# Optimization experiments

Measured on AMD Instinct MI355X. Metric: run time of the kernel, lower is better.

## Reference

```python
import jax, jax.numpy as jnp
import numpy as np

N = 4096; TD = 768; ID = 512; H = 256; NH = 4; HD = H // NH; NC = 3; E = 131072


def _gcn(x, w, b, src, dst, n):
    # GCNConv: add self loops, sym-normalize, aggregate at dst
    loop = jnp.arange(n)
    s = jnp.concatenate([src, loop])
    d = jnp.concatenate([dst, loop])
    deg = jax.ops.segment_sum(jnp.ones(s.shape[0], x.dtype), d, num_segments=n)
    dinv = jnp.where(deg > 0, jax.lax.rsqrt(deg), 0.0)
    norm = dinv[s] * dinv[d]                      # [E+N]
    h = x @ w                                     # [N,H] transform
    out = jax.ops.segment_sum(norm[:, None] * h[s], d, num_segments=n)
    return out + b


def setup_inputs() -> dict:
    key = jax.random.key(0)
    ks = jax.random.split(key, 20)
    p = lambda k, shp, sc: jax.random.normal(k, shp, jnp.float32) * sc
    inp = {
        "text_features": jax.random.normal(ks[0], (N, TD), jnp.float32),
        "image_features": jax.random.normal(ks[1], (N, ID), jnp.float32),
        "edge_index": jax.random.randint(ks[2], (2, E), 0, N, jnp.int32),
        "text_w": p(ks[3], (TD, H), 0.02), "text_b": jnp.zeros((H,), jnp.float32),
        "image_w": p(ks[4], (ID, H), 0.02), "image_b": jnp.zeros((H,), jnp.float32),
        "wq": p(ks[5], (H, H), 0.02), "bq": jnp.zeros((H,), jnp.float32),
        "wk": p(ks[6], (H, H), 0.02), "bk": jnp.zeros((H,), jnp.float32),
        "wv": p(ks[7], (H, H), 0.02), "bv": jnp.zeros((H,), jnp.float32),
        "wo": p(ks[8], (H, H), 0.02), "bo": jnp.zeros((H,), jnp.float32),
        "gcn1_w": p(ks[9], (H, H), 0.02), "gcn1_b": jnp.zeros((H,), jnp.float32),
        "gcn2_w": p(ks[10], (H, H), 0.02), "gcn2_b": jnp.zeros((H,), jnp.float32),
        "cls_w": p(ks[11], (H, NC), 0.02), "cls_b": jnp.zeros((NC,), jnp.float32),
    }
    return inp


def reference(text_features, image_features, edge_index,
              text_w, text_b, image_w, image_b,
              wq, bq, wk, bk, wv, bv, wo, bo,
              gcn1_w, gcn1_b, gcn2_w, gcn2_b, cls_w, cls_b):
    # fused linear+relu projections, then elementwise fuse of sum
    combined = (jax.nn.relu(text_features @ text_w + text_b)
                + jax.nn.relu(image_features @ image_w + image_b))  # [N,H]
    # MHA over all nodes (seq_len=N, batch=1)
    q = (combined @ wq + bq).reshape(N, NH, HD)
    k = (combined @ wk + bk).reshape(N, NH, HD)
    v = (combined @ wv + bv).reshape(N, NH, HD)
    scores = jnp.einsum('nhd,mhd->hnm', q, k) / jnp.sqrt(jnp.float32(HD))
    attn = jax.nn.softmax(scores, axis=-1)
    o = jnp.einsum('hnm,mhd->nhd', attn, v).reshape(N, H)
    attn_out = o @ wo + bo
    # two GCN layers
    src, dst = edge_index[0], edge_index[1]
    g1 = jax.nn.relu(_gcn(attn_out, gcn1_w, gcn1_b, src, dst, N))
    g2 = _gcn(g1, gcn2_w, gcn2_b, src, dst, N)
    return g2 @ cls_w + cls_b
```

## Files before the change

### kernel.cpp

```cpp
#include <hip/hip_runtime.h>
#include <hip/hip_bf16.h>

typedef unsigned short ushort;
typedef __attribute__((ext_vector_type(8))) short short8;
typedef __attribute__((ext_vector_type(4))) short short4v;
typedef __attribute__((ext_vector_type(4))) float f32x4;

constexpr int N_  = 4096;
constexpr int TD_ = 768;
constexpr int ID_ = 512;
constexpr int H_  = 256;
constexpr int HD_ = 64;
constexpr int E_  = 131072;
constexpr int SPLITS = 8;
constexpr float QSCALE = 0.125f * 1.44269504088896f;

#define MFMA16(a, b, c) __builtin_amdgcn_mfma_f32_16x16x32_bf16(a, b, c, 0, 0, 0)

__device__ inline ushort f2bf(float x) {
    union { float f; unsigned u; } v; v.f = x;
    unsigned r = v.u + 0x7fff + ((v.u >> 16) & 1);
    return (ushort)(r >> 16);
}
__device__ inline float lo2f(unsigned u) { union { unsigned x; float f; } v; v.x = u << 16; return v.f; }
__device__ inline float hi2f(unsigned u) { union { unsigned x; float f; } v; v.x = u & 0xffff0000u; return v.f; }

__device__ inline float exp2r(float x) {
    float r;
    asm("v_exp_f32 %0, %1" : "=v"(r) : "v"(x));
    return r;
}
__device__ inline unsigned pkbf(float lo, float hi) {
    union { float f; unsigned u; } a, b; a.f = lo; b.f = hi;
    return __builtin_amdgcn_perm(b.u + 0x8000u, a.u + 0x8000u, 0x07060302u);
}

__device__ inline void gl_lds16(const void* g, void* l) {
    __builtin_amdgcn_global_load_lds((const __attribute__((address_space(1))) unsigned int*)g,
                                     (__attribute__((address_space(3))) unsigned int*)l, 16, 0, 0);
}

__device__ inline void stage64(const ushort* g, long long strideEl, ushort* lds, int w, int l) {
    int r8 = l >> 3;
    int cc = (l & 7) ^ r8;
    #pragma unroll
    for (int p = 0; p < 2; p++) {
        int row = w * 16 + p * 8 + r8;
        gl_lds16(g + (long long)row * strideEl + cc * 8, lds + (w * 16 + p * 8) * 64);
    }
}
__device__ inline int swz(int row, int kOff) {
    return row * 64 + ((((kOff >> 3) ^ (row & 7))) << 3);
}


__global__ __launch_bounds__(256) void k_init(int* __restrict__ indeg, int* __restrict__ pos) {
    int i = blockIdx.x * 256 + threadIdx.x;
    indeg[i] = 0;
    pos[i] = 0;
}

__global__ __launch_bounds__(256) void k_count(const int* __restrict__ dst, int* __restrict__ indeg) {
    int e = blockIdx.x * 256 + threadIdx.x;
    atomicAdd(&indeg[dst[e]], 1);
}

__global__ __launch_bounds__(1024) void k_scan(const int* __restrict__ indeg, int* __restrict__ offs,
                                               float* __restrict__ dinv) {
    __shared__ int sums[1024];
    int t = threadIdx.x;
    int b = t * 4;
    int a0 = indeg[b], a1 = indeg[b + 1], a2 = indeg[b + 2], a3 = indeg[b + 3];
    int s = a0 + a1 + a2 + a3;
    sums[t] = s;
    __syncthreads();
    for (int off = 1; off < 1024; off <<= 1) {
        int vv = (t >= off) ? sums[t - off] : 0;
        __syncthreads();
        sums[t] += vv;
        __syncthreads();
    }
    int excl = sums[t] - s;
    offs[b]     = excl;
    offs[b + 1] = excl + a0;
    offs[b + 2] = excl + a0 + a1;
    offs[b + 3] = excl + a0 + a1 + a2;
    dinv[b]     = 1.f / sqrtf((float)(a0 + 1));
    dinv[b + 1] = 1.f / sqrtf((float)(a1 + 1));
    dinv[b + 2] = 1.f / sqrtf((float)(a2 + 1));
    dinv[b + 3] = 1.f / sqrtf((float)(a3 + 1));
}

__global__ __launch_bounds__(256) void k_scatter(const int* __restrict__ src, const int* __restrict__ dst,
                                                 const int* __restrict__ offs, const float* __restrict__ dinv,
                                                 int* __restrict__ pos, int* __restrict__ ssrc,
                                                 float* __restrict__ sw) {
    int e = blockIdx.x * 256 + threadIdx.x;
    int s = src[e], d = dst[e];
    int p = atomicAdd(&pos[d], 1);
    int idx = offs[d] + p;
    ssrc[idx] = s;
    sw[idx] = dinv[s] * dinv[d];
}


__global__ __launch_bounds__(256) void k_prep(const float* __restrict__ text, const float* __restrict__ img,
                                              const float* __restrict__ tw, const float* __restrict__ iw,
                                              const float* __restrict__ wq, const float* __restrict__ wk,
                                              const float* __restrict__ wv, const float* __restrict__ wo,
                                              const float* __restrict__ g1w, const float* __restrict__ g2w,
                                              ushort* __restrict__ textbf, ushort* __restrict__ imgbf,
                                              ushort* __restrict__ wobf,
                                              ushort* __restrict__ twT, ushort* __restrict__ iwT,
                                              ushort* __restrict__ wqT, ushort* __restrict__ wkT,
                                              ushort* __restrict__ wvT, ushort* __restrict__ g1wT,
                                              ushort* __restrict__ g2wT) {
    __shared__ float Ts[64][65];
    const int b = blockIdx.x;
    const int t = threadIdx.x;
    if (b < 2592) {
        size_t base = ((size_t)b * 256 + t) * 8;
        const size_t TXE = (size_t)N_ * TD_, IME = (size_t)N_ * ID_;
        const float* src; ushort* dst;
        if (base < TXE) { src = text + base; dst = textbf + base; }
        else if (base < TXE + IME) { src = img + (base - TXE); dst = imgbf + (base - TXE); }
        else { src = wo + (base - TXE - IME); dst = wobf + (base - TXE - IME); }
        float4 x = *(const float4*)src;
        float4 y = *(const float4*)(src + 4);
        ushort o[8] = { f2bf(x.x), f2bf(x.y), f2bf(x.z), f2bf(x.w),
                        f2bf(y.x), f2bf(y.y), f2bf(y.z), f2bf(y.w) };
        *(short8*)dst = *(const short8*)o;
        return;
    }
    int wb = b - 2592;
    const float* src; ushort* dst; int R, tile;
    if (wb < 48)       { src = tw;  dst = twT;  R = 768; tile = wb; }
    else if (wb < 80)  { src = iw;  dst = iwT;  R = 512; tile = wb - 48; }
    else if (wb < 96)  { src = wq;  dst = wqT;  R = 256; tile = wb - 80; }
    else if (wb < 112) { src = wk;  dst = wkT;  R = 256; tile = wb - 96; }
    else if (wb < 128) { src = wv;  dst = wvT;  R = 256; tile = wb - 112; }
    else if (wb < 144) { src = g1w; dst = g1wT; R = 256; tile = wb - 128; }
    else               { src = g2w; dst = g2wT; R = 256; tile = wb - 144; }
    const int r0 = (tile >> 2) * 64, c0 = (tile & 3) * 64;
    #pragma unroll
    for (int u = 0; u < 16; u++) {
        int lin = t + u * 256;
        int r = lin >> 6, c = lin & 63;
        Ts[r][c] = src[(size_t)(r0 + r) * 256 + c0 + c];
    }
    __syncthreads();
    #pragma unroll
    for (int u = 0; u < 16; u++) {
        int lin = t + u * 256;
        int c = lin >> 6, r = lin & 63;
        dst[(size_t)(c0 + c) * R + r0 + r] = f2bf(Ts[r][c]);
    }
}


__global__ __launch_bounds__(256) void k_foldw(const ushort* __restrict__ g1wT, const ushort* __restrict__ wobf,
                                               const float* __restrict__ bo,
                                               ushort* __restrict__ WpT, float* __restrict__ bp) {
    __shared__ ushort As[2][4096];
    __shared__ ushort Bs[2][4096];
    __shared__ ushort Cs[64 * 72];
    const int t = threadIdx.x;
    if (blockIdx.x == 16) {
        float acc = 0.f;
        const ushort* row = g1wT + (size_t)t * 256;
        for (int m8 = 0; m8 < 256; m8 += 8) {
            #pragma unroll
            for (int j = 0; j < 8; j++) acc += bo[m8 + j] * lo2f(((unsigned)row[m8 + j]) << 16);
        }
        bp[t] = acc;
        return;
    }
    const int bm = (blockIdx.x >> 2) * 64, bn = (blockIdx.x & 3) * 64;
    const int w = t >> 6, l = t & 63, q = l >> 4, i = l & 15;
    f32x4 acc[4];
    #pragma unroll
    for (int nt = 0; nt < 4; nt++) acc[nt] = (f32x4){0, 0, 0, 0};
    stage64(g1wT + (size_t)bm * H_, H_, As[0], w, l);
    stage64(wobf + (size_t)bn * H_, H_, Bs[0], w, l);
    for (int c = 0; c < 4; c++) {
        __syncthreads();
        if (c < 3) {
            stage64(g1wT + (size_t)bm * H_ + (c + 1) * 64, H_, As[(c + 1) & 1], w, l);
            stage64(wobf + (size_t)bn * H_ + (c + 1) * 64, H_, Bs[(c + 1) & 1], w, l);
        }
        const ushort* Ab = As[c & 1];
        const ushort* Bb = Bs[c & 1];
        #pragma unroll
        for (int kb = 0; kb < 2; kb++) {
            short8 af = *(const short8*)&Ab[swz(w * 16 + i, kb * 32 + q * 8)];
            #pragma unroll
            for (int nt = 0; nt < 4; nt++) {
                short8 bfr = *(const short8*)&Bb[swz(nt * 16 + i, kb * 32 + q * 8)];
                acc[nt] = MFMA16(af, bfr, acc[nt]);
            }
        }
    }
    __syncthreads();
    #pragma unroll
    for (int nt = 0; nt < 4; nt++)
        #pragma unroll
        for (int r = 0; r < 4; r++)
            Cs[(w * 16 + q * 4 + r) * 72 + nt * 16 + i] = f2bf(acc[nt][r]);
    __syncthreads();
    int rr = t >> 2, c16 = (t & 3) * 16;
    short8 v0 = *(const short8*)&Cs[rr * 72 + c16];
    short8 v1 = *(const short8*)&Cs[rr * 72 + c16 + 8];
    ushort* dst = WpT + (size_t)(bm + rr) * H_ + bn + c16;
    *(short8*)dst = v0;
    *(short8*)(dst + 8) = v1;
}


__global__ __launch_bounds__(256) void k_combined_mfma(const ushort* __restrict__ text, const ushort* __restrict__ img,
                                                       const ushort* __restrict__ twT, const ushort* __restrict__ iwT,
                                                       const float* __restrict__ tb, const float* __restrict__ ib,
                                                       ushort* __restrict__ out) {
    __shared__ ushort As[2][64 * 64];
    __shared__ ushort Bs[2][64 * 64];
    __shared__ ushort Cs[64 * 72];
    const int bm = blockIdx.x * 64, bn = blockIdx.y * 64;
    const int t = threadIdx.x, w = t >> 6, l = t & 63, q = l >> 4, i = l & 15;
    constexpr int NCH = 20;

    auto stageC = [&](int c, int buf) {
        if (c < 12) {
            stage64(text + (size_t)bm * TD_ + c * 64, TD_, As[buf], w, l);
            stage64(twT + (size_t)bn * TD_ + c * 64, TD_, Bs[buf], w, l);
        } else {
            int cc = c - 12;
            stage64(img + (size_t)bm * ID_ + cc * 64, ID_, As[buf], w, l);
            stage64(iwT + (size_t)bn * ID_ + cc * 64, ID_, Bs[buf], w, l);
        }
    };

    f32x4 acc1[4], acc2[4];
    #pragma unroll
    for (int nt = 0; nt < 4; nt++) { acc1[nt] = (f32x4){0,0,0,0}; acc2[nt] = (f32x4){0,0,0,0}; }

    stageC(0, 0);
    for (int c = 0; c < NCH; c++) {
        __syncthreads();
        if (c + 1 < NCH) stageC(c + 1, (c + 1) & 1);
        const ushort* Ab = As[c & 1];
        const ushort* Bb = Bs[c & 1];
        f32x4* acc = (c < 12) ? acc1 : acc2;
        #pragma unroll
        for (int kb = 0; kb < 2; kb++) {
            short8 af = *(const short8*)&Ab[swz(w * 16 + i, kb * 32 + q * 8)];
            #pragma unroll
            for (int nt = 0; nt < 4; nt++) {
                short8 bfr = *(const short8*)&Bb[swz(nt * 16 + i, kb * 32 + q * 8)];
                acc[nt] = MFMA16(af, bfr, acc[nt]);
            }
        }
    }
    __syncthreads();
    #pragma unroll
    for (int nt = 0; nt < 4; nt++) {
        float b1 = tb[bn + nt * 16 + i], b2 = ib[bn + nt * 16 + i];
        #pragma unroll
        for (int r = 0; r < 4; r++) {
            float v = fmaxf(acc1[nt][r] + b1, 0.f) + fmaxf(acc2[nt][r] + b2, 0.f);
            Cs[(w * 16 + q * 4 + r) * 72 + nt * 16 + i] = f2bf(v);
        }
    }
    __syncthreads();
    int rr = t >> 2, c16 = (t & 3) * 16;
    short8 v0 = *(const short8*)&Cs[rr * 72 + c16];
    short8 v1 = *(const short8*)&Cs[rr * 72 + c16 + 8];
    ushort* dst = out + (size_t)(bm + rr) * H_ + bn + c16;
    *(short8*)dst = v0;
    *(short8*)(dst + 8) = v1;
}


__global__ __launch_bounds__(256) void k_qkv_mfma(const ushort* __restrict__ A,
                                                  const ushort* __restrict__ WqT, const ushort* __restrict__ WkT,
                                                  const ushort* __restrict__ WvT,
                                                  const float* __restrict__ bq, const float* __restrict__ bk,
                                                  const float* __restrict__ bv,
                                                  ushort* __restrict__ Qg, ushort* __restrict__ Kg,
                                                  ushort* __restrict__ Vtg) {
    __shared__ ushort As[2][64 * 64];
    __shared__ ushort Bs[2][64 * 64];
    __shared__ ushort Cs[64 * 72];
    const int bm = blockIdx.x * 64, head = blockIdx.y, z = blockIdx.z;
    const ushort* WT = (z == 0) ? WqT : (z == 1) ? WkT : WvT;
    const float* bias = (z == 0) ? bq : (z == 1) ? bk : bv;
    const int t = threadIdx.x, w = t >> 6, l = t & 63, q = l >> 4, i = l & 15;
    f32x4 acc[4];
    #pragma unroll
    for (int nt = 0; nt < 4; nt++) acc[nt] = (f32x4){0,0,0,0};

    stage64(A + (size_t)bm * H_, H_, As[0], w, l);
    stage64(WT + (size_t)(head * 64) * H_, H_, Bs[0], w, l);
    for (int c = 0; c < 4; c++) {
        __syncthreads();
        if (c < 3) {
            stage64(A + (size_t)bm * H_ + (c + 1) * 64, H_, As[(c + 1) & 1], w, l);
            stage64(WT + (size_t)(head * 64) * H_ + (c + 1) * 64, H_, Bs[(c + 1) & 1], w, l);
        }
        const ushort* Ab = As[c & 1];
        const ushort* Bb = Bs[c & 1];
        #pragma unroll
        for (int kb = 0; kb < 2; kb++) {
            short8 af = *(const short8*)&Ab[swz(w * 16 + i, kb * 32 + q * 8)];
            #pragma unroll
            for (int nt = 0; nt < 4; nt++) {
                short8 bfr = *(const short8*)&Bb[swz(nt * 16 + i, kb * 32 + q * 8)];
                acc[nt] = MFMA16(af, bfr, acc[nt]);
            }
        }
    }
    __syncthreads();
    #pragma unroll
    for (int nt = 0; nt < 4; nt++) {
        float bv_ = bias[head * 64 + nt * 16 + i];
        #pragma unroll
        for (int r = 0; r < 4; r++) {
            float v = acc[nt][r] + bv_;
            if (z == 0) v *= QSCALE;
            if (z < 2) Cs[(w * 16 + q * 4 + r) * 72 + nt * 16 + i] = f2bf(v);
            else       Cs[(nt * 16 + i) * 72 + w * 16 + q * 4 + r] = f2bf(v);
        }
    }
    __syncthreads();
    int rr = t >> 2, c16 = (t & 3) * 16;
    short8 v0 = *(const short8*)&Cs[rr * 72 + c16];
    short8 v1 = *(const short8*)&Cs[rr * 72 + c16 + 8];
    ushort* dst;
    if (z < 2) dst = ((z == 0) ? Qg : Kg) + (size_t)head * N_ * HD_ + (size_t)(bm + rr) * HD_ + c16;
    else       dst = Vtg + (size_t)head * HD_ * N_ + (size_t)rr * N_ + bm + c16;
    *(short8*)dst = v0;
    *(short8*)(dst + 8) = v1;
}


__global__ __launch_bounds__(256) void k_attn_mfma(const ushort* __restrict__ Qg, const ushort* __restrict__ Kg,
                                                   const ushort* __restrict__ Vtg, ushort* __restrict__ Op,
                                                   float* __restrict__ lp) {
    __shared__ ushort Ks[4096];
    __shared__ ushort Vs[4096];
    __shared__ ushort Ps[4][16 * 72];
    const int head = blockIdx.y, r0 = blockIdx.x * 64, z = blockIdx.z;
    const int t = threadIdx.x, w = t >> 6, l = t & 63, q = l >> 4, i = l & 15;
    const int rw = (i ^ (i >> 1)) & 7;
    ushort* Pw = &Ps[w][0];

    short8 qf[2];
    #pragma unroll
    for (int kb = 0; kb < 2; kb++)
        qf[kb] = *(const short8*)(Qg + ((size_t)head * N_ + r0 + w * 16 + i) * HD_ + kb * 32 + q * 8);

    f32x4 Oacc[4];
    float lacc = 0.f;
    #pragma unroll
    for (int dt = 0; dt < 4; dt++) Oacc[dt] = (f32x4){0, 0, 0, 0};

    const int NT = 64 / SPLITS;
    const int cb0 = z * NT;
    for (int it = 0; it < NT; it++) {
        const int cb = cb0 + it;
        __syncthreads();
        stage64(Kg + ((size_t)head * N_ + (size_t)cb * 64) * HD_, HD_, Ks, w, l);
        stage64(Vtg + (size_t)head * HD_ * N_ + cb * 64, N_, Vs, w, l);
        __syncthreads();

        f32x4 St[4];
        #pragma unroll
        for (int kt = 0; kt < 4; kt++) St[kt] = (f32x4){0, 0, 0, 0};
        #pragma unroll
        for (int kb = 0; kb < 2; kb++) {
            #pragma unroll
            for (int kt = 0; kt < 4; kt++) {
                short8 kf = *(const short8*)&Ks[swz(kt * 16 + i, kb * 32 + q * 8)];
                St[kt] = MFMA16(kf, qf[kb], St[kt]);
            }
        }

        #pragma unroll
        for (int kt = 0; kt < 4; kt++) {
            float p0 = exp2r(St[kt][0]), p1 = exp2r(St[kt][1]);
            float p2 = exp2r(St[kt][2]), p3 = exp2r(St[kt][3]);
            lacc += (p0 + p1) + (p2 + p3);
            int off = i * 72 + (((2 * kt + (q >> 1)) ^ rw) << 3) + ((q & 1) << 2);
            uint2 v; v.x = pkbf(p0, p1); v.y = pkbf(p2, p3);
            *(uint2*)&Pw[off] = v;
        }

        #pragma unroll
        for (int kb = 0; kb < 2; kb++) {
            short8 pf = *(const short8*)&Pw[i * 72 + (((4 * kb + q) ^ rw) << 3)];
            #pragma unroll
            for (int dt = 0; dt < 4; dt++) {
                short8 vf = *(const short8*)&Vs[swz(dt * 16 + i, kb * 32 + q * 8)];
                Oacc[dt] = MFMA16(vf, pf, Oacc[dt]);
            }
        }
    }

    lacc += __shfl_xor(lacc, 16);
    lacc += __shfl_xor(lacc, 32);

    const size_t sh = ((size_t)z * 4 + head) * N_;
    const int row = r0 + w * 16 + i;
    #pragma unroll
    for (int dt = 0; dt < 4; dt++) {
        uint2 v;
        v.x = pkbf(Oacc[dt][0], Oacc[dt][1]);
        v.y = pkbf(Oacc[dt][2], Oacc[dt][3]);
        *(uint2*)&Op[(sh + row) * HD_ + dt * 16 + q * 4] = v;
    }
    if (l < 16) lp[sh + r0 + w * 16 + l] = lacc;
}

__global__ __launch_bounds__(256) void k_attn_merge(const ushort* __restrict__ Op, const float* __restrict__ lp,
                                                    ushort* __restrict__ obuf) {
    const int t = threadIdx.x;
    const int idx = blockIdx.x * 16 + (t >> 4);
    const int h = idx >> 12, n = idx & 4095;
    const int d4 = (t & 15) * 4;
    float lsum = 0.f;
    float acc[4] = {0.f, 0.f, 0.f, 0.f};
    #pragma unroll
    for (int s = 0; s < SPLITS; s++) {
        size_t sh = ((size_t)s * 4 + h) * N_ + n;
        lsum += lp[sh];
        uint2 o4 = *(const uint2*)&Op[sh * HD_ + d4];
        acc[0] += lo2f(o4.x); acc[1] += hi2f(o4.x);
        acc[2] += lo2f(o4.y); acc[3] += hi2f(o4.y);
    }
    float inv = 1.f / lsum;
    uint2 res;
    res.x = pkbf(acc[0] * inv, acc[1] * inv);
    res.y = pkbf(acc[2] * inv, acc[3] * inv);
    *(uint2*)&obuf[(size_t)n * H_ + h * HD_ + d4] = res;
}


template <bool BIAS>
__global__ __launch_bounds__(256) void k_gemm_bf16(const ushort* __restrict__ A, const ushort* __restrict__ BT,
                                                   const float* __restrict__ bias, ushort* __restrict__ outb) {
    __shared__ ushort As[2][4096];
    __shared__ ushort Bs[2][4096];
    __shared__ ushort Cs[64 * 72];
    const int bm = blockIdx.x * 64, bn = blockIdx.y * 64;
    const int t = threadIdx.x, w = t >> 6, l = t & 63, q = l >> 4, i = l & 15;
    f32x4 acc[4];
    #pragma unroll
    for (int nt = 0; nt < 4; nt++) acc[nt] = (f32x4){0, 0, 0, 0};

    stage64(A + (size_t)bm * H_, H_, As[0], w, l);
    stage64(BT + (size_t)bn * H_, H_, Bs[0], w, l);
    for (int c = 0; c < 4; c++) {
        __syncthreads();
        if (c < 3) {
            stage64(A + (size_t)bm * H_ + (c + 1) * 64, H_, As[(c + 1) & 1], w, l);
            stage64(BT + (size_t)bn * H_ + (c + 1) * 64, H_, Bs[(c + 1) & 1], w, l);
        }
        const ushort* Ab = As[c & 1];
        const ushort* Bb = Bs[c & 1];
        #pragma unroll
        for (int kb = 0; kb < 2; kb++) {
            short8 af = *(const short8*)&Ab[swz(w * 16 + i, kb * 32 + q * 8)];
            #pragma unroll
            for (int nt = 0; nt < 4; nt++) {
                short8 bfr = *(const short8*)&Bb[swz(nt * 16 + i, kb * 32 + q * 8)];
                acc[nt] = MFMA16(af, bfr, acc[nt]);
            }
        }
    }
    __syncthreads();
    #pragma unroll
    for (int nt = 0; nt < 4; nt++) {
        float bb = BIAS ? bias[bn + nt * 16 + i] : 0.f;
        #pragma unroll
        for (int r = 0; r < 4; r++)
            Cs[(w * 16 + q * 4 + r) * 72 + nt * 16 + i] = f2bf(acc[nt][r] + bb);
    }
    __syncthreads();
    int rr = t >> 2, c16 = (t & 3) * 16;
    short8 v0 = *(const short8*)&Cs[rr * 72 + c16];
    short8 v1 = *(const short8*)&Cs[rr * 72 + c16 + 8];
    ushort* dst = outb + (size_t)(bm + rr) * H_ + bn + c16;
    *(short8*)dst = v0;
    *(short8*)(dst + 8) = v1;
}


__global__ __launch_bounds__(256) void k_agg1(const ushort* __restrict__ h, const int* __restrict__ ssrc,
                                              const float* __restrict__ sw, const int* __restrict__ offs,
                                              const int* __restrict__ indeg, const float* __restrict__ dinv,
                                              const float* __restrict__ bias, ushort* __restrict__ outb) {
    const int t = threadIdx.x;
    const int j = blockIdx.x * 4 + (t >> 6);
    const int d0 = (t & 63) * 4;
    float dj = dinv[j];
    uint2 hv = *(const uint2*)&h[(size_t)j * H_ + d0];
    float s2 = dj * dj;
    float a0 = s2 * lo2f(hv.x), a1 = s2 * hi2f(hv.x), a2 = s2 * lo2f(hv.y), a3 = s2 * hi2f(hv.y);
    int start = offs[j], cnt = indeg[j];
    for (int e = 0; e < cnt; e++) {
        int s = ssrc[start + e];
        float wg = sw[start + e];
        uint2 v = *(const uint2*)&h[(size_t)s * H_ + d0];
        a0 += wg * lo2f(v.x); a1 += wg * hi2f(v.x);
        a2 += wg * lo2f(v.y); a3 += wg * hi2f(v.y);
    }
    a0 = fmaxf(a0 + bias[d0], 0.f);
    a1 = fmaxf(a1 + bias[d0 + 1], 0.f);
    a2 = fmaxf(a2 + bias[d0 + 2], 0.f);
    a3 = fmaxf(a3 + bias[d0 + 3], 0.f);
    uint2 o;
    o.x = pkbf(a0, a1);
    o.y = pkbf(a2, a3);
    *(uint2*)&outb[(size_t)j * H_ + d0] = o;
}


__global__ __launch_bounds__(256) void k_aggcls(const ushort* __restrict__ h, const int* __restrict__ ssrc,
                                                const float* __restrict__ sw, const int* __restrict__ offs,
                                                const int* __restrict__ indeg, const float* __restrict__ dinv,
                                                const float* __restrict__ bias, const float* __restrict__ cw,
                                                const float* __restrict__ cb, float* __restrict__ out) {
    const int t = threadIdx.x;
    const int j = blockIdx.x * 4 + (t >> 6);
    const int lane = t & 63;
    const int d0 = lane * 4;
    float dj = dinv[j];
    uint2 hv = *(const uint2*)&h[(size_t)j * H_ + d0];
    float s2 = dj * dj;
    float a0 = s2 * lo2f(hv.x), a1 = s2 * hi2f(hv.x), a2 = s2 * lo2f(hv.y), a3 = s2 * hi2f(hv.y);
    int start = offs[j], cnt = indeg[j];
    for (int e = 0; e < cnt; e++) {
        int s = ssrc[start + e];
        float wg = sw[start + e];
        uint2 v = *(const uint2*)&h[(size_t)s * H_ + d0];
        a0 += wg * lo2f(v.x); a1 += wg * hi2f(v.x);
        a2 += wg * lo2f(v.y); a3 += wg * hi2f(v.y);
    }
    a0 += bias[d0]; a1 += bias[d0 + 1]; a2 += bias[d0 + 2]; a3 += bias[d0 + 3];
    float p0 = 0.f, p1 = 0.f, p2 = 0.f;
    #pragma unroll
    for (int r = 0; r < 4; r++) {
        float g = (r == 0) ? a0 : (r == 1) ? a1 : (r == 2) ? a2 : a3;
        p0 += g * cw[(d0 + r) * 3 + 0];
        p1 += g * cw[(d0 + r) * 3 + 1];
        p2 += g * cw[(d0 + r) * 3 + 2];
    }
    #pragma unroll
    for (int off = 32; off > 0; off >>= 1) {
        p0 += __shfl_xor(p0, off);
        p1 += __shfl_xor(p1, off);
        p2 += __shfl_xor(p2, off);
    }
    if (lane == 0) {
        out[j * 3 + 0] = p0 + cb[0];
        out[j * 3 + 1] = p1 + cb[1];
        out[j * 3 + 2] = p2 + cb[2];
    }
}


extern "C" void kernel_launch(void* const* d_in, const int* in_sizes, int n_in,
                              void* d_out, int out_size, void* d_ws, size_t ws_size,
                              hipStream_t stream) {
    const float* text = (const float*)d_in[0];
    const float* img  = (const float*)d_in[1];
    const int*   eidx = (const int*)d_in[2];
    const float* tw  = (const float*)d_in[3];
    const float* tb  = (const float*)d_in[4];
    const float* iw  = (const float*)d_in[5];
    const float* ib  = (const float*)d_in[6];
    const float* wq  = (const float*)d_in[7];
    const float* bq  = (const float*)d_in[8];
    const float* wk  = (const float*)d_in[9];
    const float* bk  = (const float*)d_in[10];
    const float* wv  = (const float*)d_in[11];
    const float* bv  = (const float*)d_in[12];
    const float* wo  = (const float*)d_in[13];
    const float* bo  = (const float*)d_in[14];
    const float* g1w = (const float*)d_in[15];
    const float* g1b = (const float*)d_in[16];
    const float* g2w = (const float*)d_in[17];
    const float* g2b = (const float*)d_in[18];
    const float* cw  = (const float*)d_in[19];
    const float* cbv = (const float*)d_in[20];

    char* W = (char*)d_ws;
    size_t cur = 0;
    auto alloc = [&](size_t sz) { char* p = W + cur; cur += (sz + 255) & ~(size_t)255; return p; };

    float* dinv  = (float*)alloc(N_ * 4);
    float* swv   = (float*)alloc(E_ * 4);
    int* indeg   = (int*)alloc(N_ * 4);
    int* offs    = (int*)alloc(N_ * 4);
    int* pos     = (int*)alloc(N_ * 4);
    int* ssrc    = (int*)alloc(E_ * 4);
    ushort* Qg   = (ushort*)alloc((size_t)N_ * H_ * 2);
    ushort* Kg   = (ushort*)alloc((size_t)N_ * H_ * 2);
    ushort* Vtg  = (ushort*)alloc((size_t)N_ * H_ * 2);
    ushort* obuf = (ushort*)alloc((size_t)N_ * H_ * 2);
    ushort* WpT  = (ushort*)alloc((size_t)H_ * H_ * 2);
    float* bp    = (float*)alloc(H_ * 4);
    ushort* g1wT = (ushort*)alloc((size_t)H_ * H_ * 2);
    ushort* g2wT = (ushort*)alloc((size_t)H_ * H_ * 2);
    ushort* wobf = (ushort*)alloc((size_t)H_ * H_ * 2);
    float* lp    = (float*)alloc((size_t)SPLITS * 4 * N_ * 4);
    char* S = W + cur;

    ushort* textbf = (ushort*)S;
    ushort* imgbf  = textbf + (size_t)N_ * TD_;
    ushort* twT    = imgbf + (size_t)N_ * ID_;
    ushort* iwT    = twT + (size_t)TD_ * H_;
    ushort* wqT    = iwT + (size_t)ID_ * H_;
    ushort* wkT    = wqT + (size_t)H_ * H_;
    ushort* wvT    = wkT + (size_t)H_ * H_;
    ushort* combbf = wvT + (size_t)H_ * H_;
    ushort* Op = (ushort*)S;
    ushort* hbuf  = (ushort*)S;
    ushort* g1b16 = (ushort*)(S + (size_t)2 * 1024 * 1024);
    ushort* hbuf2 = (ushort*)(S + (size_t)4 * 1024 * 1024);

    const int* esrc = eidx;
    const int* edst = eidx + E_;

    k_init<<<dim3(N_ / 256), dim3(256), 0, stream>>>(indeg, pos);
    k_count<<<dim3(E_ / 256), dim3(256), 0, stream>>>(edst, indeg);
    k_scan<<<dim3(1), dim3(1024), 0, stream>>>(indeg, offs, dinv);
    k_scatter<<<dim3(E_ / 256), dim3(256), 0, stream>>>(esrc, edst, offs, dinv, pos, ssrc, swv);

    k_prep<<<dim3(2752), dim3(256), 0, stream>>>(text, img, tw, iw, wq, wk, wv, wo, g1w, g2w,
                                                 textbf, imgbf, wobf, twT, iwT, wqT, wkT, wvT, g1wT, g2wT);
    k_foldw<<<dim3(17), dim3(256), 0, stream>>>(g1wT, wobf, bo, WpT, bp);

    k_combined_mfma<<<dim3(64, 4), dim3(256), 0, stream>>>(textbf, imgbf, twT, iwT, tb, ib, combbf);
    k_qkv_mfma<<<dim3(64, 4, 3), dim3(256), 0, stream>>>(combbf, wqT, wkT, wvT, bq, bk, bv, Qg, Kg, Vtg);
    k_attn_mfma<<<dim3(64, 4, SPLITS), dim3(256), 0, stream>>>(Qg, Kg, Vtg, Op, lp);
    k_attn_merge<<<dim3(1024), dim3(256), 0, stream>>>(Op, lp, obuf);

    k_gemm_bf16<true><<<dim3(64, 4), dim3(256), 0, stream>>>(obuf, WpT, bp, hbuf);
    k_agg1<<<dim3(N_ / 4), dim3(256), 0, stream>>>(hbuf, ssrc, swv, offs, indeg, dinv, g1b, g1b16);
    k_gemm_bf16<false><<<dim3(64, 4), dim3(256), 0, stream>>>(g1b16, g2wT, nullptr, hbuf2);
    k_aggcls<<<dim3(N_ / 4), dim3(256), 0, stream>>>(hbuf2, ssrc, swv, offs, indeg, dinv, g2b, cw, cbv,
                                                     (float*)d_out);
}
```

Before: 256.1 us.

## Replace multi-kernel pipeline with single persistent megakernel using grid barriers

Merges all stages (bf16 conversion, weight transposes, degree counting, CSR build, projections, QKV, attention, GCN GEMMs and aggregation) into one persistent kernel of 256 blocks. Stages are separated by a software grid barrier on an atomic counter instead of kernel launches. Graph preprocessing is overlapped with the projection GEMM, and the attention split-K merge and Wo/GCN1 weight folding appear to be dropped in favour of separate GEMMs. This removes launch gaps but limits attention and GEMM parallelism to 256 blocks at one block per CU, and the spin barrier depends on all blocks being co-resident.

Measured after the change: 501.7 us. 95.9% more time.

```diff
diff --git a/kernel.cpp b/kernel.cpp
--- a/kernel.cpp
+++ b/kernel.cpp
@@ -3,7 +3,6 @@
 
 typedef unsigned short ushort;
 typedef __attribute__((ext_vector_type(8))) short short8;
-typedef __attribute__((ext_vector_type(4))) short short4v;
 typedef __attribute__((ext_vector_type(4))) float f32x4;
 
 constexpr int N_  = 4096;
@@ -12,7 +11,6 @@
 constexpr int H_  = 256;
 constexpr int HD_ = 64;
 constexpr int E_  = 131072;
-constexpr int SPLITS = 8;
 constexpr float QSCALE = 0.125f * 1.44269504088896f;
 
 #define MFMA16(a, b, c) __builtin_amdgcn_mfma_f32_16x16x32_bf16(a, b, c, 0, 0, 0)
@@ -53,516 +51,412 @@
     return row * 64 + ((((kOff >> 3) ^ (row & 7))) << 3);
 }
 
-
-__global__ __launch_bounds__(256) void k_init(int* __restrict__ indeg, int* __restrict__ pos) {
-    int i = blockIdx.x * 256 + threadIdx.x;
-    indeg[i] = 0;
-    pos[i] = 0;
-}
-
-__global__ __launch_bounds__(256) void k_count(const int* __restrict__ dst, int* __restrict__ indeg) {
-    int e = blockIdx.x * 256 + threadIdx.x;
-    atomicAdd(&indeg[dst[e]], 1);
-}
-
-__global__ __launch_bounds__(1024) void k_scan(const int* __restrict__ indeg, int* __restrict__ offs,
-                                               float* __restrict__ dinv) {
-    __shared__ int sums[1024];
-    int t = threadIdx.x;
-    int b = t * 4;
-    int a0 = indeg[b], a1 = indeg[b + 1], a2 = indeg[b + 2], a3 = indeg[b + 3];
-    int s = a0 + a1 + a2 + a3;
-    sums[t] = s;
+union SharedU {
+    struct { ushort A[2][4096]; ushort B[2][4096]; ushort C[4608]; } g;
+    struct { ushort K[2][4096]; ushort V[2][4096]; ushort P[4][1152]; } a;
+    struct { float T[64][65]; } p;
+    struct { int sums[256]; } s;
+};
+
+struct Params {
+    const float *text, *img;
+    const int *eidx;
+    const float *tw, *tb, *iw, *ib, *wq, *bq, *wk, *bk, *wv, *bv, *wo, *bo;
+    const float *g1w, *g1b, *g2w, *g2b, *cw, *cb;
+    float* out;
+    unsigned* bar;
+    float *dinv, *swv;
+    int *indeg, *offs, *pos, *ssrc;
+    ushort *textbf, *imgbf, *twT, *iwT, *wqT, *wkT, *wvT, *woT, *g1wT, *g2wT;
+    ushort *combbf, *Qg, *Kg, *Vtg, *obuf, *attn_out, *hbuf, *g1b16, *hbuf2;
+};
+
+__device__ inline void gridbar(unsigned* bar) {
     __syncthreads();
-    for (int off = 1; off < 1024; off <<= 1) {
-        int vv = (t >= off) ? sums[t - off] : 0;
+    if (threadIdx.x == 0) {
+        __threadfence();
+        unsigned tk = __hip_atomic_fetch_add(bar, 1u, __ATOMIC_ACQ_REL, __HIP_MEMORY_SCOPE_AGENT);
+        unsigned target = (tk / 256u + 1u) * 256u;
+        while (__hip_atomic_load(bar, __ATOMIC_ACQUIRE, __HIP_MEMORY_SCOPE_AGENT) < target)
+            __builtin_amdgcn_s_sleep(1);
+    }
+    __syncthreads();
+}
+
+__global__ __launch_bounds__(256, 1) void mega(Params P) {
+    __shared__ SharedU sh;
+    const int bid = blockIdx.x, t = threadIdx.x;
+    const int w = t >> 6, l = t & 63, q = l >> 4, i = l & 15;
+    const int* esrc = P.eidx;
+    const int* edst = P.eidx + E_;
+
+    for (int u = bid; u < 2752; u += 256) {
+        if (u < 2560) {
+            size_t base = ((size_t)u * 256 + t) * 8;
+            const size_t TXE = (size_t)N_ * TD_;
+            const float* src; ushort* dst;
+            if (base < TXE) { src = P.text + base; dst = P.textbf + base; }
+            else            { src = P.img + (base - TXE); dst = P.imgbf + (base - TXE); }
+            float4 x = *(const float4*)src;
+            float4 y = *(const float4*)(src + 4);
+            ushort o[8] = { f2bf(x.x), f2bf(x.y), f2bf(x.z), f2bf(x.w),
+                            f2bf(y.x), f2bf(y.y), f2bf(y.z), f2bf(y.w) };
+            *(short8*)dst = *(const short8*)o;
+        } else if (u < 2736) {
+            int wb = u - 2560;
+            const float* src; ushort* dst; int R, tile;
+            if (wb < 48)       { src = P.tw;  dst = P.twT;  R = 768; tile = wb; }
+            else if (wb < 80)  { src = P.iw;  dst = P.iwT;  R = 512; tile = wb - 48; }
+            else if (wb < 96)  { src = P.wq;  dst = P.wqT;  R = 256; tile = wb - 80; }
+            else if (wb < 112) { src = P.wk;  dst = P.wkT;  R = 256; tile = wb - 96; }
+            else if (wb < 128) { src = P.wv;  dst = P.wvT;  R = 256; tile = wb - 112; }
+            else if (wb < 144) { src = P.wo;  dst = P.woT;  R = 256; tile = wb - 128; }
+            else if (wb < 160) { src = P.g1w; dst = P.g1wT; R = 256; tile = wb - 144; }
+            else               { src = P.g2w; dst = P.g2wT; R = 256; tile = wb - 160; }
+            const int r0 = (tile >> 2) * 64, c0 = (tile & 3) * 64;
+            __syncthreads();
+            #pragma unroll
+            for (int uu = 0; uu < 16; uu++) {
+                int lin = t + uu * 256;
+                int r = lin >> 6, c = lin & 63;
+                sh.p.T[r][c] = src[(size_t)(r0 + r) * 256 + c0 + c];
+            }
+            __syncthreads();
+            #pragma unroll
+            for (int uu = 0; uu < 16; uu++) {
+                int lin = t + uu * 256;
+                int c = lin >> 6, r = lin & 63;
+                dst[(size_t)(c0 + c) * R + r0 + r] = f2bf(sh.p.T[r][c]);
+            }
+        } else {
+            int zi = u - 2736;
+            if (zi < 4) {
+                int* d0 = (zi < 2) ? P.indeg + zi * 2048 : P.pos + (zi - 2) * 2048;
+                #pragma unroll
+                for (int k2 = 0; k2 < 8; k2++) d0[t * 8 + k2] = 0;
+            }
+        }
+    }
+    gridbar(P.bar);
+
+    {
+        int e = bid * 512 + t;
+        atomicAdd(&P.indeg[edst[e]], 1);
+        atomicAdd(&P.indeg[edst[e + 256]], 1);
+    }
+    {
+        const int bm = (bid >> 2) * 64, bn = (bid & 3) * 64;
+        constexpr int NCH = 20;
+        auto stageC = [&](int c, int buf) {
+            if (c < 12) {
+                stage64(P.textbf + (size_t)bm * TD_ + c * 64, TD_, sh.g.A[buf], w, l);
+                stage64(P.twT + (size_t)bn * TD_ + c * 64, TD_, sh.g.B[buf], w, l);
+            } else {
+                int cc = c - 12;
+                stage64(P.imgbf + (size_t)bm * ID_ + cc * 64, ID_, sh.g.A[buf], w, l);
+                stage64(P.iwT + (size_t)bn * ID_ + cc * 64, ID_, sh.g.B[buf], w, l);
+            }
+        };
+        f32x4 acc1[4], acc2[4];
+        #pragma unroll
+        for (int nt = 0; nt < 4; nt++) { acc1[nt] = (f32x4){0,0,0,0}; acc2[nt] = (f32x4){0,0,0,0}; }
+        stageC(0, 0);
+        for (int c = 0; c < NCH; c++) {
+            __syncthreads();
+            if (c + 1 < NCH) stageC(c + 1, (c + 1) & 1);
+            const ushort* Ab = sh.g.A[c & 1];
+            const ushort* Bb = sh.g.B[c & 1];
+            f32x4* acc = (c < 12) ? acc1 : acc2;
+            #pragma unroll
+            for (int kb = 0; kb < 2; kb++) {
+                short8 af = *(const short8*)&Ab[swz(w * 16 + i, kb * 32 + q * 8)];
+                #pragma unroll
+                for (int nt = 0; nt < 4; nt++) {
+                    short8 bfr = *(const short8*)&Bb[swz(nt * 16 + i, kb * 32 + q * 8)];
+                    acc[nt] = MFMA16(af, bfr, acc[nt]);
+                }
+            }
+        }
         __syncthreads();
-        sums[t] += vv;
+        #pragma unroll
+        for (int nt = 0; nt < 4; nt++) {
+            float b1 = P.tb[bn + nt * 16 + i], b2 = P.ib[bn + nt * 16 + i];
+            #pragma unroll
+            for (int r = 0; r < 4; r++) {
+                float v = fmaxf(acc1[nt][r] + b1, 0.f) + fmaxf(acc2[nt][r] + b2, 0.f);
+                sh.g.C[(w * 16 + q * 4 + r) * 72 + nt * 16 + i] = f2bf(v);
+            }
+        }
         __syncthreads();
-    }
-    int excl = sums[t] - s;
-    offs[b]     = excl;
-    offs[b + 1] = excl + a0;
-    offs[b + 2] = excl + a0 + a1;
-    offs[b + 3] = excl + a0 + a1 + a2;
-    dinv[b]     = 1.f / sqrtf((float)(a0 + 1));
-    dinv[b + 1] = 1.f / sqrtf((float)(a1 + 1));
-    dinv[b + 2] = 1.f / sqrtf((float)(a2 + 1));
-    dinv[b + 3] = 1.f / sqrtf((float)(a3 + 1));
-}
-
-__global__ __launch_bounds__(256) void k_scatter(const int* __restrict__ src, const int* __restrict__ dst,
-                                                 const int* __restrict__ offs, const float* __restrict__ dinv,
-                                                 int* __restrict__ pos, int* __restrict__ ssrc,
-                                                 float* __restrict__ sw) {
-    int e = blockIdx.x * 256 + threadIdx.x;
-    int s = src[e], d = dst[e];
-    int p = atomicAdd(&pos[d], 1);
-    int idx = offs[d] + p;
-    ssrc[idx] = s;
-    sw[idx] = dinv[s] * dinv[d];
-}
-
-
-__global__ __launch_bounds__(256) void k_prep(const float* __restrict__ text, const float* __restrict__ img,
-                                              const float* __restrict__ tw, const float* __restrict__ iw,
-                                              const float* __restrict__ wq, const float* __restrict__ wk,
-                                              const float* __restrict__ wv, const float* __restrict__ wo,
-                                              const float* __restrict__ g1w, const float* __restrict__ g2w,
-                                              ushort* __restrict__ textbf, ushort* __restrict__ imgbf,
-                                              ushort* __restrict__ wobf,
-                                              ushort* __restrict__ twT, ushort* __restrict__ iwT,
-                                              ushort* __restrict__ wqT, ushort* __restrict__ wkT,
-                                              ushort* __restrict__ wvT, ushort* __restrict__ g1wT,
-                                              ushort* __restrict__ g2wT) {
-    __shared__ float Ts[64][65];
-    const int b = blockIdx.x;
-    const int t = threadIdx.x;
-    if (b < 2592) {
-        size_t base = ((size_t)b * 256 + t) * 8;
-        const size_t TXE = (size_t)N_ * TD_, IME = (size_t)N_ * ID_;
-        const float* src; ushort* dst;
-        if (base < TXE) { src = text + base; dst = textbf + base; }
-        else if (base < TXE + IME) { src = img + (base - TXE); dst = imgbf + (base - TXE); }
-        else { src = wo + (base - TXE - IME); dst = wobf + (base - TXE - IME); }
-        float4 x = *(const float4*)src;
-        float4 y = *(const float4*)(src + 4);
-        ushort o[8] = { f2bf(x.x), f2bf(x.y), f2bf(x.z), f2bf(x.w),
-                        f2bf(y.x), f2bf(y.y), f2bf(y.z), f2bf(y.w) };
-        *(short8*)dst = *(const short8*)o;
-        return;
-    }
-    int wb = b - 2592;
-    const float* src; ushort* dst; int R, tile;
-    if (wb < 48)       { src = tw;  dst = twT;  R = 768; tile = wb; }
-    else if (wb < 80)  { src = iw;  dst = iwT;  R = 512; tile = wb - 48; }
-    else if (wb < 96)  { src = wq;  dst = wqT;  R = 256; tile = wb - 80; }
-    else if (wb < 112) { src = wk;  dst = wkT;  R = 256; tile = wb - 96; }
-    else if (wb < 128) { src = wv;  dst = wvT;  R = 256; tile = wb - 112; }
-    else if (wb < 144) { src = g1w; dst = g1wT; R = 256; tile = wb - 128; }
-    else               { src = g2w; dst = g2wT; R = 256; tile = wb - 144; }
-    const int r0 = (tile >> 2) * 64, c0 = (tile & 3) * 64;
-    #pragma unroll
-    for (int u = 0; u < 16; u++) {
-        int lin = t + u * 256;
-        int r = lin >> 6, c = lin & 63;
-        Ts[r][c] = src[(size_t)(r0 + r) * 256 + c0 + c];
-    }
-    __syncthreads();
-    #pragma unroll
-    for (int u = 0; u < 16; u++) {
-        int lin = t + u * 256;
-        int c = lin >> 6, r = lin & 63;
-        dst[(size_t)(c0 + c) * R + r0 + r] = f2bf(Ts[r][c]);
-    }
-}
-
-
-__global__ __launch_bounds__(256) void k_foldw(const ushort* __restrict__ g1wT, const ushort* __restrict__ wobf,
-                                               const float* __restrict__ bo,
-                                               ushort* __restrict__ WpT, float* __restrict__ bp) {
-    __shared__ ushort As[2][4096];
-    __shared__ ushort Bs[2][4096];
-    __shared__ ushort Cs[64 * 72];
-    const int t = threadIdx.x;
-    if (blockIdx.x == 16) {
-        float acc = 0.f;
-        const ushort* row = g1wT + (size_t)t * 256;
-        for (int m8 = 0; m8 < 256; m8 += 8) {
-            #pragma unroll
-            for (int j = 0; j < 8; j++) acc += bo[m8 + j] * lo2f(((unsigned)row[m8 + j]) << 16);
-        }
-        bp[t] = acc;
-        return;
-    }
-    const int bm = (blockIdx.x >> 2) * 64, bn = (blockIdx.x & 3) * 64;
-    const int w = t >> 6, l = t & 63, q = l >> 4, i = l & 15;
-    f32x4 acc[4];
-    #pragma unroll
-    for (int nt = 0; nt < 4; nt++) acc[nt] = (f32x4){0, 0, 0, 0};
-    stage64(g1wT + (size_t)bm * H_, H_, As[0], w, l);
-    stage64(wobf + (size_t)bn * H_, H_, Bs[0], w, l);
-    for (int c = 0; c < 4; c++) {
+        int rr = t >> 2, c16 = (t & 3) * 16;
+        short8 v0 = *(const short8*)&sh.g.C[rr * 72 + c16];
+        short8 v1 = *(const short8*)&sh.g.C[rr * 72 + c16 + 8];
+        ushort* dst = P.combbf + (size_t)(bm + rr) * H_ + bn + c16;
+        *(short8*)dst = v0;
+        *(short8*)(dst + 8) = v1;
+    }
+    gridbar(P.bar);
+
+    {
+        const int bm = (bid >> 2) * 64, head = bid & 3;
+        for (int z = 0; z < 3; z++) {
+            const ushort* WT = (z == 0) ? P.wqT : (z == 1) ? P.wkT : P.wvT;
+            const float* bias = (z == 0) ? P.bq : (z == 1) ? P.bk : P.bv;
+            f32x4 acc[4];
+            #pragma unroll
+            for (int nt = 0; nt < 4; nt++) acc[nt] = (f32x4){0,0,0,0};
+            stage64(P.combbf + (size_t)bm * H_, H_, sh.g.A[0], w, l);
+            stage64(WT + (size_t)(head * 64) * H_, H_, sh.g.B[0], w, l);
+            for (int c = 0; c < 4; c++) {
+                __syncthreads();
+                if (c < 3) {
+                    stage64(P.combbf + (size_t)bm * H_ + (c + 1) * 64, H_, sh.g.A[(c + 1) & 1], w, l);
+                    stage64(WT + (size_t)(head * 64) * H_ + (c + 1) * 64, H_, sh.g.B[(c + 1) & 1], w, l);
+                }
+                const ushort* Ab = sh.g.A[c & 1];
+                const ushort* Bb = sh.g.B[c & 1];
+                #pragma unroll
+                for (int kb = 0; kb < 2; kb++) {
+                    short8 af = *(const short8*)&Ab[swz(w * 16 + i, kb * 32 + q * 8)];
+                    #pragma unroll
+                    for (int nt = 0; nt < 4; nt++) {
+                        short8 bfr = *(const short8*)&Bb[swz(nt * 16 + i, kb * 32 + q * 8)];
+                        acc[nt] = MFMA16(af, bfr, acc[nt]);
+                    }
+                }
+            }
+            __syncthreads();
+            #pragma unroll
+            for (int nt = 0; nt < 4; nt++) {
+                float bv_ = bias[head * 64 + nt * 16 + i];
+                #pragma unroll
+                for (int r = 0; r < 4; r++) {
+                    float v = acc[nt][r] + bv_;
+                    if (z == 0) v *= QSCALE;
+                    if (z < 2) sh.g.C[(w * 16 + q * 4 + r) * 72 + nt * 16 + i] = f2bf(v);
+                    else       sh.g.C[(nt * 16 + i) * 72 + w * 16 + q * 4 + r] = f2bf(v);
+                }
+            }
+            __syncthreads();
+            int rr = t >> 2, c16 = (t & 3) * 16;
+            short8 v0 = *(const short8*)&sh.g.C[rr * 72 + c16];
+            short8 v1 = *(const short8*)&sh.g.C[rr * 72 + c16 + 8];
+            ushort* dst;
+            if (z < 2) dst = ((z == 0) ? P.Qg : P.Kg) + (size_t)head * N_ * HD_ + (size_t)(bm + rr) * HD_ + c16;
+            else       dst = P.Vtg + (size_t)head * HD_ * N_ + (size_t)rr * N_ + bm + c16;
+            *(short8*)dst = v0;
+            *(short8*)(dst + 8) = v1;
+        }
+    }
+    if (bid == 0) {
         __syncthreads();
-        if (c < 3) {
-            stage64(g1wT + (size_t)bm * H_ + (c + 1) * 64, H_, As[(c + 1) & 1], w, l);
-            stage64(wobf + (size_t)bn * H_ + (c + 1) * 64, H_, Bs[(c + 1) & 1], w, l);
-        }
-        const ushort* Ab = As[c & 1];
-        const ushort* Bb = Bs[c & 1];
-        #pragma unroll
-        for (int kb = 0; kb < 2; kb++) {
-            short8 af = *(const short8*)&Ab[swz(w * 16 + i, kb * 32 + q * 8)];
-            #pragma unroll
-            for (int nt = 0; nt < 4; nt++) {
-                short8 bfr = *(const short8*)&Bb[swz(nt * 16 + i, kb * 32 + q * 8)];
-                acc[nt] = MFMA16(af, bfr, acc[nt]);
-            }
-        }
-    }
-    __syncthreads();
-    #pragma unroll
-    for (int nt = 0; nt < 4; nt++)
-        #pragma unroll
-        for (int r = 0; r < 4; r++)
-            Cs[(w * 16 + q * 4 + r) * 72 + nt * 16 + i] = f2bf(acc[nt][r]);
-    __syncthreads();
-    int rr = t >> 2, c16 = (t & 3) * 16;
-    short8 v0 = *(const short8*)&Cs[rr * 72 + c16];
-    short8 v1 = *(const short8*)&Cs[rr * 72 + c16 + 8];
-    ushort* dst = WpT + (size_t)(bm + rr) * H_ + bn + c16;
-    *(short8*)dst = v0;
-    *(short8*)(dst + 8) = v1;
-}
-
-
-__global__ __launch_bounds__(256) void k_combined_mfma(const ushort* __restrict__ text, const ushort* __restrict__ img,
-                                                       const ushort* __restrict__ twT, const ushort* __restrict__ iwT,
-                                                       const float* __restrict__ tb, const float* __restrict__ ib,
-                                                       ushort* __restrict__ out) {
-    __shared__ ushort As[2][64 * 64];
-    __shared__ ushort Bs[2][64 * 64];
-    __shared__ ushort Cs[64 * 72];
-    const int bm = blockIdx.x * 64, bn = blockIdx.y * 64;
-    const int t = threadIdx.x, w = t >> 6, l = t & 63, q = l >> 4, i = l & 15;
-    constexpr int NCH = 20;
-
-    auto stageC = [&](int c, int buf) {
-        if (c < 12) {
-            stage64(text + (size_t)bm * TD_ + c * 64, TD_, As[buf], w, l);
-            stage64(twT + (size_t)bn * TD_ + c * 64, TD_, Bs[buf], w, l);
-        } else {
-            int cc = c - 12;
-            stage64(img + (size_t)bm * ID_ + cc * 64, ID_, As[buf], w, l);
-            stage64(iwT + (size_t)bn * ID_ + cc * 64, ID_, Bs[buf], w, l);
-        }
+        int v[16]; int ssum = 0; int base = t * 16;
+        #pragma unroll
+        for (int k2 = 0; k2 < 16; k2++) { v[k2] = P.indeg[base + k2]; ssum += v[k2]; }
+        sh.s.sums[t] = ssum;
+        __syncthreads();
+        for (int off = 1; off < 256; off <<= 1) {
+            int x = (t >= off) ? sh.s.sums[t - off] : 0;
+            __syncthreads();
+            sh.s.sums[t] += x;
+            __syncthreads();
+        }
+        int excl = sh.s.sums[t] - ssum;
+        #pragma unroll
+        for (int k2 = 0; k2 < 16; k2++) {
+            P.offs[base + k2] = excl;
+            excl += v[k2];
+            P.dinv[base + k2] = 1.f / sqrtf((float)(v[k2] + 1));
+        }
+    }
+    gridbar(P.bar);
+
+    {
+        #pragma unroll
+        for (int rep = 0; rep < 2; rep++) {
+            int ee = bid * 512 + t + rep * 256;
+            int s = esrc[ee], d = edst[ee];
+            int p_ = atomicAdd(&P.pos[d], 1);
+            int idx = P.offs[d] + p_;
+            P.ssrc[idx] = s;
+            P.swv[idx] = P.dinv[s] * P.dinv[d];
+        }
+    }
+    {
+        const int head = bid & 3, r0 = (bid >> 2) * 64;
+        const int rw = (i ^ (i >> 1)) & 7;
+        ushort* Pw = &sh.a.P[w][0];
+        short8 qf[2];
+        #pragma unroll
+        for (int kb = 0; kb < 2; kb++)
+            qf[kb] = *(const short8*)(P.Qg + ((size_t)head * N_ + r0 + w * 16 + i) * HD_ + kb * 32 + q * 8);
+        f32x4 Oacc[4];
+        float lacc = 0.f;
+        #pragma unroll
+        for (int dt = 0; dt < 4; dt++) Oacc[dt] = (f32x4){0, 0, 0, 0};
+
+        stage64(P.Kg + (size_t)head * N_ * HD_, HD_, sh.a.K[0], w, l);
+        stage64(P.Vtg + (size_t)head * HD_ * N_, N_, sh.a.V[0], w, l);
+        for (int it = 0; it < 64; it++) {
+            __syncthreads();
+            if (it + 1 < 64) {
+                stage64(P.Kg + ((size_t)head * N_ + (size_t)(it + 1) * 64) * HD_, HD_, sh.a.K[(it + 1) & 1], w, l);
+                stage64(P.Vtg + (size_t)head * HD_ * N_ + (it + 1) * 64, N_, sh.a.V[(it + 1) & 1], w, l);
+            }
+            const ushort* Kb = sh.a.K[it & 1];
+            const ushort* Vb = sh.a.V[it & 1];
+
+            f32x4 St[4];
+            #pragma unroll
+            for (int kt = 0; kt < 4; kt++) St[kt] = (f32x4){0, 0, 0, 0};
+            #pragma unroll
+            for (int kb = 0; kb < 2; kb++) {
+                #pragma unroll
+                for (int kt = 0; kt < 4; kt++) {
+                    short8 kf = *(const short8*)&Kb[swz(kt * 16 + i, kb * 32 + q * 8)];
+                    St[kt] = MFMA16(kf, qf[kb], St[kt]);
+                }
+            }
+            #pragma unroll
+            for (int kt = 0; kt < 4; kt++) {
+                float p0 = exp2r(St[kt][0]), p1 = exp2r(St[kt][1]);
+                float p2 = exp2r(St[kt][2]), p3 = exp2r(St[kt][3]);
+                lacc += (p0 + p1) + (p2 + p3);
+                int off = i * 72 + (((2 * kt + (q >> 1)) ^ rw) << 3) + ((q & 1) << 2);
+                uint2 v; v.x = pkbf(p0, p1); v.y = pkbf(p2, p3);
+                *(uint2*)&Pw[off] = v;
+            }
+            #pragma unroll
+            for (int kb = 0; kb < 2; kb++) {
+                short8 pf = *(const short8*)&Pw[i * 72 + (((4 * kb + q) ^ rw) << 3)];
+                #pragma unroll
+                for (int dt = 0; dt < 4; dt++) {
+                    short8 vf = *(const short8*)&Vb[swz(dt * 16 + i, kb * 32 + q * 8)];
+                    Oacc[dt] = MFMA16(vf, pf, Oacc[dt]);
+                }
+            }
+        }
+        lacc += __shfl_xor(lacc, 16);
+        lacc += __shfl_xor(lacc, 32);
+        float inv = 1.f / lacc;
+        const int row = r0 + w * 16 + i;
+        #pragma unroll
+        for (int dt = 0; dt < 4; dt++) {
+            uint2 v;
+            v.x = pkbf(Oacc[dt][0] * inv, Oacc[dt][1] * inv);
+            v.y = pkbf(Oacc[dt][2] * inv, Oacc[dt][3] * inv);
+            *(uint2*)&P.obuf[(size_t)row * H_ + head * HD_ + dt * 16 + q * 4] = v;
+        }
+    }
+    gridbar(P.bar);
+
+    auto gemmP = [&](const ushort* A, const ushort* BT, const float* bias, ushort* outb) {
+        const int bm = (bid >> 2) * 64, bn = (bid & 3) * 64;
+        f32x4 acc[4];
+        #pragma unroll
+        for (int nt = 0; nt < 4; nt++) acc[nt] = (f32x4){0, 0, 0, 0};
+        stage64(A + (size_t)bm * H_, H_, sh.g.A[0], w, l);
+        stage64(BT + (size_t)bn * H_, H_, sh.g.B[0], w, l);
+        for (int c = 0; c < 4; c++) {
+            __syncthreads();
+            if (c < 3) {
+                stage64(A + (size_t)bm * H_ + (c + 1) * 64, H_, sh.g.A[(c + 1) & 1], w, l);
+                stage64(BT + (size_t)bn * H_ + (c + 1) * 64, H_, sh.g.B[(c + 1) & 1], w, l);
+            }
+            const ushort* Ab = sh.g.A[c & 1];
+            const ushort* Bb = sh.g.B[c & 1];
+            #pragma unroll
+            for (int kb = 0; kb < 2; kb++) {
+                short8 af = *(const short8*)&Ab[swz(w * 16 + i, kb * 32 + q * 8)];
+                #pragma unroll
+                for (int nt = 0; nt < 4; nt++) {
+                    short8 bfr = *(const short8*)&Bb[swz(nt * 16 + i, kb * 32 + q * 8)];
+                    acc[nt] = MFMA16(af, bfr, acc[nt]);
+                }
+            }
+        }
+        __syncthreads();
+        #pragma unroll
+        for (int nt = 0; nt < 4; nt++) {
+            float bb = bias ? bias[bn + nt * 16 + i] : 0.f;
+            #pragma unroll
+            for (int r = 0; r < 4; r++)
+                sh.g.C[(w * 16 + q * 4 + r) * 72 + nt * 16 + i] = f2bf(acc[nt][r] + bb);
+        }
+        __syncthreads();
+        int rr = t >> 2, c16 = (t & 3) * 16;
+        short8 v0 = *(const short8*)&sh.g.C[rr * 72 + c16];
+        short8 v1 = *(const short8*)&sh.g.C[rr * 72 + c16 + 8];
+        ushort* dst = outb + (size_t)(bm + rr) * H_ + bn + c16;
+        *(short8*)dst = v0;
+        *(short8*)(dst + 8) = v1;
     };
 
-    f32x4 acc1[4], acc2[4];
-    #pragma unroll
-    for (int nt = 0; nt < 4; nt++) { acc1[nt] = (f32x4){0,0,0,0}; acc2[nt] = (f32x4){0,0,0,0}; }
-
-    stageC(0, 0);
-    for (int c = 0; c < NCH; c++) {
-        __syncthreads();
-        if (c + 1 < NCH) stageC(c + 1, (c + 1) & 1);
-        const ushort* Ab = As[c & 1];
-        const ushort* Bb = Bs[c & 1];
-        f32x4* acc = (c < 12) ? acc1 : acc2;
-        #pragma unroll
-        for (int kb = 0; kb < 2; kb++) {
-            short8 af = *(const short8*)&Ab[swz(w * 16 + i, kb * 32 + q * 8)];
-            #pragma unroll
-            for (int nt = 0; nt < 4; nt++) {
-                short8 bfr = *(const short8*)&Bb[swz(nt * 16 + i, kb * 32 + q * 8)];
-                acc[nt] = MFMA16(af, bfr, acc[nt]);
-            }
-        }
-    }
-    __syncthreads();
-    #pragma unroll
-    for (int nt = 0; nt < 4; nt++) {
-        float b1 = tb[bn + nt * 16 + i], b2 = ib[bn + nt * 16 + i];
-        #pragma unroll
-        for (int r = 0; r < 4; r++) {
-            float v = fmaxf(acc1[nt][r] + b1, 0.f) + fmaxf(acc2[nt][r] + b2, 0.f);
-            Cs[(w * 16 + q * 4 + r) * 72 + nt * 16 + i] = f2bf(v);
-        }
-    }
-    __syncthreads();
-    int rr = t >> 2, c16 = (t & 3) * 16;
-    short8 v0 = *(const short8*)&Cs[rr * 72 + c16];
-    short8 v1 = *(const short8*)&Cs[rr * 72 + c16 + 8];
-    ushort* dst = out + (size_t)(bm + rr) * H_ + bn + c16;
-    *(short8*)dst = v0;
-    *(short8*)(dst + 8) = v1;
-}
-
-
-__global__ __launch_bounds__(256) void k_qkv_mfma(const ushort* __restrict__ A,
-                                                  const ushort* __restrict__ WqT, const ushort* __restrict__ WkT,
-                                                  const ushort* __restrict__ WvT,
-                                                  const float* __restrict__ bq, const float* __restrict__ bk,
-                                                  const float* __restrict__ bv,
-                                                  ushort* __restrict__ Qg, ushort* __restrict__ Kg,
-                                                  ushort* __restrict__ Vtg) {
-    __shared__ ushort As[2][64 * 64];
-    __shared__ ushort Bs[2][64 * 64];
-    __shared__ ushort Cs[64 * 72];
-    const int bm = blockIdx.x * 64, head = blockIdx.y, z = blockIdx.z;
-    const ushort* WT = (z == 0) ? WqT : (z == 1) ? WkT : WvT;
-    const float* bias = (z == 0) ? bq : (z == 1) ? bk : bv;
-    const int t = threadIdx.x, w = t >> 6, l = t & 63, q = l >> 4, i = l & 15;
-    f32x4 acc[4];
-    #pragma unroll
-    for (int nt = 0; nt < 4; nt++) acc[nt] = (f32x4){0,0,0,0};
-
-    stage64(A + (size_t)bm * H_, H_, As[0], w, l);
-    stage64(WT + (size_t)(head * 64) * H_, H_, Bs[0], w, l);
-    for (int c = 0; c < 4; c++) {
-        __syncthreads();
-        if (c < 3) {
-            stage64(A + (size_t)bm * H_ + (c + 1) * 64, H_, As[(c + 1) & 1], w, l);
-            stage64(WT + (size_t)(head * 64) * H_ + (c + 1) * 64, H_, Bs[(c + 1) & 1], w, l);
-        }
-        const ushort* Ab = As[c & 1];
-        const ushort* Bb = Bs[c & 1];
-        #pragma unroll
-        for (int kb = 0; kb < 2; kb++) {
-            short8 af = *(const short8*)&Ab[swz(w * 16 + i, kb * 32 + q * 8)];
-            #pragma unroll
-            for (int nt = 0; nt < 4; nt++) {
-                short8 bfr = *(const short8*)&Bb[swz(nt * 16 + i, kb * 32 + q * 8)];
-                acc[nt] = MFMA16(af, bfr, acc[nt]);
-            }
-        }
-    }
-    __syncthreads();
-    #pragma unroll
-    for (int nt = 0; nt < 4; nt++) {
-        float bv_ = bias[head * 64 + nt * 16 + i];
-        #pragma unroll
-        for (int r = 0; r < 4; r++) {
-            float v = acc[nt][r] + bv_;
-            if (z == 0) v *= QSCALE;
-            if (z < 2) Cs[(w * 16 + q * 4 + r) * 72 + nt * 16 + i] = f2bf(v);
-            else       Cs[(nt * 16 + i) * 72 + w * 16 + q * 4 + r] = f2bf(v);
-        }
-    }
-    __syncthreads();
-    int rr = t >> 2, c16 = (t & 3) * 16;
-    short8 v0 = *(const short8*)&Cs[rr * 72 + c16];
-    short8 v1 = *(const short8*)&Cs[rr * 72 + c16 + 8];
-    ushort* dst;
-    if (z < 2) dst = ((z == 0) ? Qg : Kg) + (size_t)head * N_ * HD_ + (size_t)(bm + rr) * HD_ + c16;
-    else       dst = Vtg + (size_t)head * HD_ * N_ + (size_t)rr * N_ + bm + c16;
-    *(short8*)dst = v0;
-    *(short8*)(dst + 8) = v1;
-}
-
-
-__global__ __launch_bounds__(256) void k_attn_mfma(const ushort* __restrict__ Qg, const ushort* __restrict__ Kg,
-                                                   const ushort* __restrict__ Vtg, ushort* __restrict__ Op,
-                                                   float* __restrict__ lp) {
-    __shared__ ushort Ks[4096];
-    __shared__ ushort Vs[4096];
-    __shared__ ushort Ps[4][16 * 72];
-    const int head = blockIdx.y, r0 = blockIdx.x * 64, z = blockIdx.z;
-    const int t = threadIdx.x, w = t >> 6, l = t & 63, q = l >> 4, i = l & 15;
-    const int rw = (i ^ (i >> 1)) & 7;
-    ushort* Pw = &Ps[w][0];
-
-    short8 qf[2];
-    #pragma unroll
-    for (int kb = 0; kb < 2; kb++)
-        qf[kb] = *(const short8*)(Qg + ((size_t)head * N_ + r0 + w * 16 + i) * HD_ + kb * 32 + q * 8);
-
-    f32x4 Oacc[4];
-    float lacc = 0.f;
-    #pragma unroll
-    for (int dt = 0; dt < 4; dt++) Oacc[dt] = (f32x4){0, 0, 0, 0};
-
-    const int NT = 64 / SPLITS;
-    const int cb0 = z * NT;
-    for (int it = 0; it < NT; it++) {
-        const int cb = cb0 + it;
-        __syncthreads();
-        stage64(Kg + ((size_t)head * N_ + (size_t)cb * 64) * HD_, HD_, Ks, w, l);
-        stage64(Vtg + (size_t)head * HD_ * N_ + cb * 64, N_, Vs, w, l);
-        __syncthreads();
-
-        f32x4 St[4];
-        #pragma unroll
-        for (int kt = 0; kt < 4; kt++) St[kt] = (f32x4){0, 0, 0, 0};
-        #pragma unroll
-        for (int kb = 0; kb < 2; kb++) {
-            #pragma unroll
-            for (int kt = 0; kt < 4; kt++) {
-                short8 kf = *(const short8*)&Ks[swz(kt * 16 + i, kb * 32 + q * 8)];
-                St[kt] = MFMA16(kf, qf[kb], St[kt]);
-            }
-        }
-
-        #pragma unroll
-        for (int kt = 0; kt < 4; kt++) {
-            float p0 = exp2r(St[kt][0]), p1 = exp2r(St[kt][1]);
-            float p2 = exp2r(St[kt][2]), p3 = exp2r(St[kt][3]);
-            lacc += (p0 + p1) + (p2 + p3);
-            int off = i * 72 + (((2 * kt + (q >> 1)) ^ rw) << 3) + ((q & 1) << 2);
-            uint2 v; v.x = pkbf(p0, p1); v.y = pkbf(p2, p3);
-            *(uint2*)&Pw[off] = v;
-        }
-
-        #pragma unroll
-        for (int kb = 0; kb < 2; kb++) {
-            short8 pf = *(const short8*)&Pw[i * 72 + (((4 * kb + q) ^ rw) << 3)];
-            #pragma unroll
-            for (int dt = 0; dt < 4; dt++) {
-                short8 vf = *(const short8*)&Vs[swz(dt * 16 + i, kb * 32 + q * 8)];
-                Oacc[dt] = MFMA16(vf, pf, Oacc[dt]);
-            }
-        }
-    }
-
-    lacc += __shfl_xor(lacc, 16);
-    lacc += __shfl_xor(lacc, 32);
-
-    const size_t sh = ((size_t)z * 4 + head) * N_;
-    const int row = r0 + w * 16 + i;
-    #pragma unroll
-    for (int dt = 0; dt < 4; dt++) {
-        uint2 v;
-        v.x = pkbf(Oacc[dt][0], Oacc[dt][1]);
-        v.y = pkbf(Oacc[dt][2], Oacc[dt][3]);
-        *(uint2*)&Op[(sh + row) * HD_ + dt * 16 + q * 4] = v;
-    }
-    if (l < 16) lp[sh + r0 + w * 16 + l] = lacc;
-}
-
-__global__ __launch_bounds__(256) void k_attn_merge(const ushort* __restrict__ Op, const float* __restrict__ lp,
-                                                    ushort* __restrict__ obuf) {
-    const int t = threadIdx.x;
-    const int idx = blockIdx.x * 16 + (t >> 4);
-    const int h = idx >> 12, n = idx & 4095;
-    const int d4 = (t & 15) * 4;
-    float lsum = 0.f;
-    float acc[4] = {0.f, 0.f, 0.f, 0.f};
-    #pragma unroll
-    for (int s = 0; s < SPLITS; s++) {
-        size_t sh = ((size_t)s * 4 + h) * N_ + n;
-        lsum += lp[sh];
-        uint2 o4 = *(const uint2*)&Op[sh * HD_ + d4];
-        acc[0] += lo2f(o4.x); acc[1] += hi2f(o4.x);
-        acc[2] += lo2f(o4.y); acc[3] += hi2f(o4.y);
-    }
-    float inv = 1.f / lsum;
-    uint2 res;
-    res.x = pkbf(acc[0] * inv, acc[1] * inv);
-    res.y = pkbf(acc[2] * inv, acc[3] * inv);
-    *(uint2*)&obuf[(size_t)n * H_ + h * HD_ + d4] = res;
-}
-
-
-template <bool BIAS>
-__global__ __launch_bounds__(256) void k_gemm_bf16(const ushort* __restrict__ A, const ushort* __restrict__ BT,
-                                                   const float* __restrict__ bias, ushort* __restrict__ outb) {
-    __shared__ ushort As[2][4096];
-    __shared__ ushort Bs[2][4096];
-    __shared__ ushort Cs[64 * 72];
-    const int bm = blockIdx.x * 64, bn = blockIdx.y * 64;
-    const int t = threadIdx.x, w = t >> 6, l = t & 63, q = l >> 4, i = l & 15;
-    f32x4 acc[4];
-    #pragma unroll
-    for (int nt = 0; nt < 4; nt++) acc[nt] = (f32x4){0, 0, 0, 0};
-
-    stage64(A + (size_t)bm * H_, H_, As[0], w, l);
-    stage64(BT + (size_t)bn * H_, H_, Bs[0], w, l);
-    for (int c = 0; c < 4; c++) {
-        __syncthreads();
-        if (c < 3) {
-            stage64(A + (size_t)bm * H_ + (c + 1) * 64, H_, As[(c + 1) & 1], w, l);
-            stage64(BT + (size_t)bn * H_ + (c + 1) * 64, H_, Bs[(c + 1) & 1], w, l);
-        }
-        const ushort* Ab = As[c & 1];
-        const ushort* Bb = Bs[c & 1];
-        #pragma unroll
-        for (int kb = 0; kb < 2; kb++) {
-            short8 af = *(const short8*)&Ab[swz(w * 16 + i, kb * 32 + q * 8)];
-            #pragma unroll
-            for (int nt = 0; nt < 4; nt++) {
-                short8 bfr = *(const short8*)&Bb[swz(nt * 16 + i, kb * 32 + q * 8)];
-                acc[nt] = MFMA16(af, bfr, acc[nt]);
-            }
-        }
-    }
-    __syncthreads();
-    #pragma unroll
-    for (int nt = 0; nt < 4; nt++) {
-        float bb = BIAS ? bias[bn + nt * 16 + i] : 0.f;
-        #pragma unroll
-        for (int r = 0; r < 4; r++)
-            Cs[(w * 16 + q * 4 + r) * 72 + nt * 16 + i] = f2bf(acc[nt][r] + bb);
-    }
-    __syncthreads();
-    int rr = t >> 2, c16 = (t & 3) * 16;
-    short8 v0 = *(const short8*)&Cs[rr * 72 + c16];
-    short8 v1 = *(const short8*)&Cs[rr * 72 + c16 + 8];
-    ushort* dst = outb + (size_t)(bm + rr) * H_ + bn + c16;
-    *(short8*)dst = v0;
-    *(short8*)(dst + 8) = v1;
-}
-
-
-__global__ __launch_bounds__(256) void k_agg1(const ushort* __restrict__ h, const int* __restrict__ ssrc,
-                                              const float* __restrict__ sw, const int* __restrict__ offs,
-                                              const int* __restrict__ indeg, const float* __restrict__ dinv,
-                                              const float* __restrict__ bias, ushort* __restrict__ outb) {
-    const int t = threadIdx.x;
-    const int j = blockIdx.x * 4 + (t >> 6);
-    const int d0 = (t & 63) * 4;
-    float dj = dinv[j];
-    uint2 hv = *(const uint2*)&h[(size_t)j * H_ + d0];
-    float s2 = dj * dj;
-    float a0 = s2 * lo2f(hv.x), a1 = s2 * hi2f(hv.x), a2 = s2 * lo2f(hv.y), a3 = s2 * hi2f(hv.y);
-    int start = offs[j], cnt = indeg[j];
-    for (int e = 0; e < cnt; e++) {
-        int s = ssrc[start + e];
-        float wg = sw[start + e];
-        uint2 v = *(const uint2*)&h[(size_t)s * H_ + d0];
-        a0 += wg * lo2f(v.x); a1 += wg * hi2f(v.x);
-        a2 += wg * lo2f(v.y); a3 += wg * hi2f(v.y);
-    }
-    a0 = fmaxf(a0 + bias[d0], 0.f);
-    a1 = fmaxf(a1 + bias[d0 + 1], 0.f);
-    a2 = fmaxf(a2 + bias[d0 + 2], 0.f);
-    a3 = fmaxf(a3 + bias[d0 + 3], 0.f);
-    uint2 o;
-    o.x = pkbf(a0, a1);
-    o.y = pkbf(a2, a3);
-    *(uint2*)&outb[(size_t)j * H_ + d0] = o;
-}
-
-
-__global__ __launch_bounds__(256) void k_aggcls(const ushort* __restrict__ h, const int* __restrict__ ssrc,
-                                                const float* __restrict__ sw, const int* __restrict__ offs,
-                                                const int* __restrict__ indeg, const float* __restrict__ dinv,
-                                                const float* __restrict__ bias, const float* __restrict__ cw,
-                                                const float* __restrict__ cb, float* __restrict__ out) {
-    const int t = threadIdx.x;
-    const int j = blockIdx.x * 4 + (t >> 6);
-    const int lane = t & 63;
-    const int d0 = lane * 4;
-    float dj = dinv[j];
-    uint2 hv = *(const uint2*)&h[(size_t)j * H_ + d0];
-    float s2 = dj * dj;
-    float a0 = s2 * lo2f(hv.x), a1 = s2 * hi2f(hv.x), a2 = s2 * lo2f(hv.y), a3 = s2 * hi2f(hv.y);
-    int start = offs[j], cnt = indeg[j];
-    for (int e = 0; e < cnt; e++) {
-        int s = ssrc[start + e];
-        float wg = sw[start + e];
-        uint2 v = *(const uint2*)&h[(size_t)s * H_ + d0];
-        a0 += wg * lo2f(v.x); a1 += wg * hi2f(v.x);
-        a2 += wg * lo2f(v.y); a3 += wg * hi2f(v.y);
-    }
-    a0 += bias[d0]; a1 += bias[d0 + 1]; a2 += bias[d0 + 2]; a3 += bias[d0 + 3];
-    float p0 = 0.f, p1 = 0.f, p2 = 0.f;
-    #pragma unroll
-    for (int r = 0; r < 4; r++) {
-        float g = (r == 0) ? a0 : (r == 1) ? a1 : (r == 2) ? a2 : a3;
-        p0 += g * cw[(d0 + r) * 3 + 0];
-        p1 += g * cw[(d0 + r) * 3 + 1];
-        p2 += g * cw[(d0 + r) * 3 + 2];
-    }
-    #pragma unroll
-    for (int off = 32; off > 0; off >>= 1) {
-        p0 += __shfl_xor(p0, off);
-        p1 += __shfl_xor(p1, off);
-        p2 += __shfl_xor(p2, off);
-    }
-    if (lane == 0) {
-        out[j * 3 + 0] = p0 + cb[0];
-        out[j * 3 + 1] = p1 + cb[1];
-        out[j * 3 + 2] = p2 + cb[2];
+    auto gather = [&](const ushort* h, int j, float& a0, float& a1, float& a2, float& a3) {
+        const int d0 = l * 4;
+        float dj = P.dinv[j];
+        float s2 = dj * dj;
+        uint2 hv = *(const uint2*)&h[(size_t)j * H_ + d0];
+        a0 = s2 * lo2f(hv.x); a1 = s2 * hi2f(hv.x);
+        a2 = s2 * lo2f(hv.y); a3 = s2 * hi2f(hv.y);
+        int start = P.offs[j], cnt = P.indeg[j];
+        for (int e = 0; e < cnt; e++) {
+            int s = P.ssrc[start + e];
+            float wg = P.swv[start + e];
+            uint2 v = *(const uint2*)&h[(size_t)s * H_ + d0];
+            a0 += wg * lo2f(v.x); a1 += wg * hi2f(v.x);
+            a2 += wg * lo2f(v.y); a3 += wg * hi2f(v.y);
+        }
+    };
+
+    gemmP(P.obuf, P.woT, P.bo, P.attn_out);
+    gridbar(P.bar);
+    gemmP(P.attn_out, P.g1wT, nullptr, P.hbuf);
+    gridbar(P.bar);
+    {
+        #pragma unroll
+        for (int k2 = 0; k2 < 4; k2++) {
+            int j = bid * 16 + w * 4 + k2;
+            float a0, a1, a2, a3;
+            gather(P.hbuf, j, a0, a1, a2, a3);
+            const int d0 = l * 4;
+            a0 = fmaxf(a0 + P.g1b[d0], 0.f);
+            a1 = fmaxf(a1 + P.g1b[d0 + 1], 0.f);
+            a2 = fmaxf(a2 + P.g1b[d0 + 2], 0.f);
+            a3 = fmaxf(a3 + P.g1b[d0 + 3], 0.f);
+            uint2 o; o.x = pkbf(a0, a1); o.y = pkbf(a2, a3);
+            *(uint2*)&P.g1b16[(size_t)j * H_ + d0] = o;
+        }
+    }
+    gridbar(P.bar);
+    gemmP(P.g1b16, P.g2wT, nullptr, P.hbuf2);
+    gridbar(P.bar);
+    {
+        #pragma unroll
+        for (int k2 = 0; k2 < 4; k2++) {
+            int j = bid * 16 + w * 4 + k2;
+            float a0, a1, a2, a3;
+            gather(P.hbuf2, j, a0, a1, a2, a3);
+            const int d0 = l * 4;
+            a0 += P.g2b[d0]; a1 += P.g2b[d0 + 1]; a2 += P.g2b[d0 + 2]; a3 += P.g2b[d0 + 3];
+            float p0 = a0 * P.cw[d0 * 3 + 0] + a1 * P.cw[(d0 + 1) * 3 + 0]
+                     + a2 * P.cw[(d0 + 2) * 3 + 0] + a3 * P.cw[(d0 + 3) * 3 + 0];
+            float p1 = a0 * P.cw[d0 * 3 + 1] + a1 * P.cw[(d0 + 1) * 3 + 1]
+                     + a2 * P.cw[(d0 + 2) * 3 + 1] + a3 * P.cw[(d0 + 3) * 3 + 1];
+            float p2 = a0 * P.cw[d0 * 3 + 2] + a1 * P.cw[(d0 + 1) * 3 + 2]
+                     + a2 * P.cw[(d0 + 2) * 3 + 2] + a3 * P.cw[(d0 + 3) * 3 + 2];
+            #pragma unroll
+            for (int off = 32; off > 0; off >>= 1) {
+                p0 += __shfl_xor(p0, off);
+                p1 += __shfl_xor(p1, off);
+                p2 += __shfl_xor(p2, off);
+            }
+            if (l == 0) {
+                P.out[j * 3 + 0] = p0 + P.cb[0];
+                P.out[j * 3 + 1] = p1 + P.cb[1];
+                P.out[j * 3 + 2] = p2 + P.cb[2];
+            }
+        }
     }
 }
 
@@ -570,83 +464,52 @@
 extern "C" void kernel_launch(void* const* d_in, const int* in_sizes, int n_in,
                               void* d_out, int out_size, void* d_ws, size_t ws_size,
                               hipStream_t stream) {
-    const float* text = (const float*)d_in[0];
-    const float* img  = (const float*)d_in[1];
-    const int*   eidx = (const int*)d_in[2];
-    const float* tw  = (const float*)d_in[3];
-    const float* tb  = (const float*)d_in[4];
-    const float* iw  = (const float*)d_in[5];
-    const float* ib  = (const float*)d_in[6];
-    const float* wq  = (const float*)d_in[7];
-    const float* bq  = (const float*)d_in[8];
-    const float* wk  = (const float*)d_in[9];
-    const float* bk  = (const float*)d_in[10];
-    const float* wv  = (const float*)d_in[11];
-    const float* bv  = (const float*)d_in[12];
-    const float* wo  = (const float*)d_in[13];
-    const float* bo  = (const float*)d_in[14];
-    const float* g1w = (const float*)d_in[15];
-    const float* g1b = (const float*)d_in[16];
-    const float* g2w = (const float*)d_in[17];
-    const float* g2b = (const float*)d_in[18];
-    const float* cw  = (const float*)d_in[19];
-    const float* cbv = (const float*)d_in[20];
-
     char* W = (char*)d_ws;
     size_t cur = 0;
     auto alloc = [&](size_t sz) { char* p = W + cur; cur += (sz + 255) & ~(size_t)255; return p; };
 
-    float* dinv  = (float*)alloc(N_ * 4);
-    float* swv   = (float*)alloc(E_ * 4);
-    int* indeg   = (int*)alloc(N_ * 4);
-    int* offs    = (int*)alloc(N_ * 4);
-    int* pos     = (int*)alloc(N_ * 4);
-    int* ssrc    = (int*)alloc(E_ * 4);
-    ushort* Qg   = (ushort*)alloc((size_t)N_ * H_ * 2);
-    ushort* Kg   = (ushort*)alloc((size_t)N_ * H_ * 2);
-    ushort* Vtg  = (ushort*)alloc((size_t)N_ * H_ * 2);
-    ushort* obuf = (ushort*)alloc((size_t)N_ * H_ * 2);
-    ushort* WpT  = (ushort*)alloc((size_t)H_ * H_ * 2);
-    float* bp    = (float*)alloc(H_ * 4);
-    ushort* g1wT = (ushort*)alloc((size_t)H_ * H_ * 2);
-    ushort* g2wT = (ushort*)alloc((size_t)H_ * H_ * 2);
-    ushort* wobf = (ushort*)alloc((size_t)H_ * H_ * 2);
-    float* lp    = (float*)alloc((size_t)SPLITS * 4 * N_ * 4);
-    char* S = W + cur;
-
-    ushort* textbf = (ushort*)S;
-    ushort* imgbf  = textbf + (size_t)N_ * TD_;
-    ushort* twT    = imgbf + (size_t)N_ * ID_;
-    ushort* iwT    = twT + (size_t)TD_ * H_;
-    ushort* wqT    = iwT + (size_t)ID_ * H_;
-    ushort* wkT    = wqT + (size_t)H_ * H_;
-    ushort* wvT    = wkT + (size_t)H_ * H_;
-    ushort* combbf = wvT + (size_t)H_ * H_;
-    ushort* Op = (ushort*)S;
-    ushort* hbuf  = (ushort*)S;
-    ushort* g1b16 = (ushort*)(S + (size_t)2 * 1024 * 1024);
-    ushort* hbuf2 = (ushort*)(S + (size_t)4 * 1024 * 1024);
-
-    const int* esrc = eidx;
-    const int* edst = eidx + E_;
-
-    k_init<<<dim3(N_ / 256), dim3(256), 0, stream>>>(indeg, pos);
-    k_count<<<dim3(E_ / 256), dim3(256), 0, stream>>>(edst, indeg);
-    k_scan<<<dim3(1), dim3(1024), 0, stream>>>(indeg, offs, dinv);
-    k_scatter<<<dim3(E_ / 256), dim3(256), 0, stream>>>(esrc, edst, offs, dinv, pos, ssrc, swv);
-
-    k_prep<<<dim3(2752), dim3(256), 0, stream>>>(text, img, tw, iw, wq, wk, wv, wo, g1w, g2w,
-                                                 textbf, imgbf, wobf, twT, iwT, wqT, wkT, wvT, g1wT, g2wT);
-    k_foldw<<<dim3(17), dim3(256), 0, stream>>>(g1wT, wobf, bo, WpT, bp);
-
-    k_combined_mfma<<<dim3(64, 4), dim3(256), 0, stream>>>(textbf, imgbf, twT, iwT, tb, ib, combbf);
-    k_qkv_mfma<<<dim3(64, 4, 3), dim3(256), 0, stream>>>(combbf, wqT, wkT, wvT, bq, bk, bv, Qg, Kg, Vtg);
-    k_attn_mfma<<<dim3(64, 4, SPLITS), dim3(256), 0, stream>>>(Qg, Kg, Vtg, Op, lp);
-    k_attn_merge<<<dim3(1024), dim3(256), 0, stream>>>(Op, lp, obuf);
-
-    k_gemm_bf16<true><<<dim3(64, 4), dim3(256), 0, stream>>>(obuf, WpT, bp, hbuf);
-    k_agg1<<<dim3(N_ / 4), dim3(256), 0, stream>>>(hbuf, ssrc, swv, offs, indeg, dinv, g1b, g1b16);
-    k_gemm_bf16<false><<<dim3(64, 4), dim3(256), 0, stream>>>(g1b16, g2wT, nullptr, hbuf2);
-    k_aggcls<<<dim3(N_ / 4), dim3(256), 0, stream>>>(hbuf2, ssrc, swv, offs, indeg, dinv, g2b, cw, cbv,
-                                                     (float*)d_out);
-}
+    Params P;
+    P.text = (const float*)d_in[0];
+    P.img  = (const float*)d_in[1];
+    P.eidx = (const int*)d_in[2];
+    P.tw  = (const float*)d_in[3];  P.tb = (const float*)d_in[4];
+    P.iw  = (const float*)d_in[5];  P.ib = (const float*)d_in[6];
+    P.wq  = (const float*)d_in[7];  P.bq = (const float*)d_in[8];
+    P.wk  = (const float*)d_in[9];  P.bk = (const float*)d_in[10];
+    P.wv  = (const float*)d_in[11]; P.bv = (const float*)d_in[12];
+    P.wo  = (const float*)d_in[13]; P.bo = (const float*)d_in[14];
+    P.g1w = (const float*)d_in[15]; P.g1b = (const float*)d_in[16];
+    P.g2w = (const float*)d_in[17]; P.g2b = (const float*)d_in[18];
+    P.cw  = (const float*)d_in[19]; P.cb = (const float*)d_in[20];
+    P.out = (float*)d_out;
+
+    P.bar    = (unsigned*)alloc(256);
+    P.dinv   = (float*)alloc(N_ * 4);
+    P.swv    = (float*)alloc(E_ * 4);
+    P.indeg  = (int*)alloc(N_ * 4);
+    P.offs   = (int*)alloc(N_ * 4);
+    P.pos    = (int*)alloc(N_ * 4);
+    P.ssrc   = (int*)alloc(E_ * 4);
+    P.textbf = (ushort*)alloc((size_t)N_ * TD_ * 2);
+    P.imgbf  = (ushort*)alloc((size_t)N_ * ID_ * 2);
+    P.twT    = (ushort*)alloc((size_t)TD_ * H_ * 2);
+    P.iwT    = (ushort*)alloc((size_t)ID_ * H_ * 2);
+    P.wqT    = (ushort*)alloc((size_t)H_ * H_ * 2);
+    P.wkT    = (ushort*)alloc((size_t)H_ * H_ * 2);
+    P.wvT    = (ushort*)alloc((size_t)H_ * H_ * 2);
+    P.woT    = (ushort*)alloc((size_t)H_ * H_ * 2);
+    P.g1wT   = (ushort*)alloc((size_t)H_ * H_ * 2);
+    P.g2wT   = (ushort*)alloc((size_t)H_ * H_ * 2);
+    P.combbf = (ushort*)alloc((size_t)N_ * H_ * 2);
+    P.Qg     = (ushort*)alloc((size_t)N_ * H_ * 2);
+    P.Kg     = (ushort*)alloc((size_t)N_ * H_ * 2);
+    P.Vtg    = (ushort*)alloc((size_t)N_ * H_ * 2);
+    P.obuf   = (ushort*)alloc((size_t)N_ * H_ * 2);
+    P.attn_out = (ushort*)alloc((size_t)N_ * H_ * 2);
+    P.hbuf   = (ushort*)alloc((size_t)N_ * H_ * 2);
+    P.g1b16  = (ushort*)alloc((size_t)N_ * H_ * 2);
+    P.hbuf2  = (ushort*)alloc((size_t)N_ * H_ * 2);
+
+    hipMemsetAsync(P.bar, 0, sizeof(unsigned), stream);
+    mega<<<dim3(256), dim3(256), 0, stream>>>(P);
+}
```
